# Performance work log

Hardware: AMD Instinct MI355X
Metric: run time of the kernel (lower is better)

Reference implementation:

```python
import jax, jax.numpy as jnp
import numpy as np

B, N, K, D_MODEL = 4, 16384, 32, 64

def gather_neighbors(x, idx):
    # x: [B, N, F], idx: [B, N, K] -> [B, N, K, F]
    return jnp.take_along_axis(x[:, :, None, :], idx[:, :, :, None], axis=1)

def setup_inputs() -> dict:
    key = jax.random.key(0)
    k1, k2, k3, k4, k5 = jax.random.split(key, 5)
    x = jax.random.normal(k1, (B, N, D_MODEL), dtype=jnp.float32)
    pos = jax.random.normal(k2, (B, N, 3), dtype=jnp.float32)
    neighbor_idx = jax.random.randint(k3, (B, N, K), 0, N, dtype=jnp.int32)
    W1 = jax.random.normal(k4, (3, D_MODEL), dtype=jnp.float32) * (1.0 / np.sqrt(3.0))
    b1 = jnp.zeros((D_MODEL,), dtype=jnp.float32)
    W2 = jax.random.normal(k5, (D_MODEL, D_MODEL), dtype=jnp.float32) * (1.0 / np.sqrt(D_MODEL))
    b2 = jnp.zeros((D_MODEL,), dtype=jnp.float32)
    return {"x": x, "pos": pos, "neighbor_idx": neighbor_idx,
            "W1": W1, "b1": b1, "W2": W2, "b2": b2}

def reference(x, pos, neighbor_idx, W1, b1, W2, b2):
    # gather neighbor positions: [B, N, K, 3]
    neighbors = gather_neighbors(pos, neighbor_idx)
    rel_pos = pos[:, :, None, :] - neighbors              # [B, N, K, 3]
    # weight MLP: Linear(3,d) + LeakyReLU(0.1), Linear(d,d)
    h = jax.nn.leaky_relu(jnp.einsum('bnkd,df->bnkf', rel_pos, W1) + b1, 0.1)
    w = jnp.einsum('bnkf,fg->bnkg', h, W2) + b2           # [B, N, K, F]
    xg = gather_neighbors(x, neighbor_idx)                # [B, N, K, F]
    return jnp.sum(w * xg, axis=2)                        # [B, N, F]
```

## Files before the change

### kernel.cpp

```cpp
#include <hip/hip_runtime.h>


#define NPTS   16384
#define KNB    32
#define F      64
#define BATCH  4
#define LOG2N  14
#define WPTS   8

typedef _Float16 h2     __attribute__((ext_vector_type(2)));
typedef _Float16 h8     __attribute__((ext_vector_type(8)));
typedef float    f32x16 __attribute__((ext_vector_type(16)));

__global__ __launch_bounds__(256, 2) void pointconv_mfma(
    const float* __restrict__ x,
    const float* __restrict__ pos,
    const int*   __restrict__ idx,
    const float* __restrict__ W1,
    const float* __restrict__ b1,
    const float* __restrict__ W2,
    const float* __restrict__ b2,
    float*       __restrict__ out)
{
    __shared__ __align__(16) _Float16 w1p[32][8];
    __shared__ __align__(16) _Float16 w2f[2][4][2][32][8];

    const int tid = threadIdx.x;
    if (tid < 32) {
        const int g = 2 * tid;
        w1p[tid][0] = (_Float16)W1[0 * F + g]; w1p[tid][1] = (_Float16)W1[0 * F + g + 1];
        w1p[tid][2] = (_Float16)W1[1 * F + g]; w1p[tid][3] = (_Float16)W1[1 * F + g + 1];
        w1p[tid][4] = (_Float16)W1[2 * F + g]; w1p[tid][5] = (_Float16)W1[2 * F + g + 1];
        w1p[tid][6] = (_Float16)b1[g];         w1p[tid][7] = (_Float16)b1[g + 1];
    }
#pragma unroll
    for (int r = 0; r < 16; ++r) {
        const int e = r * 256 + tid;
        const int g = e >> 6, f = e & 63;
        w2f[(g >> 3) & 1][g >> 4][f & 1][f >> 1][g & 7] = (_Float16)W2[e];
    }
    __syncthreads();

    const int lane = tid & 63;
    const int wv   = tid >> 6;
    const int m    = lane & 31;
    const int hf   = lane >> 5;

    h8 bfrag[4][2];
#pragma unroll
    for (int t = 0; t < 4; ++t)
#pragma unroll
        for (int c = 0; c < 2; ++c)
            bfrag[t][c] = *(const h8*)&w2f[hf][t][c][m][0];

    const float2 b2v = *(const float2*)(b2 + 2 * m);

    const int gb    = blockIdx.x;
    const int xcd   = gb & 7;
    const int q     = gb >> 3;
    const int batch = xcd >> 1;
    const int pg    = q + ((xcd & 1) << 8);
    const int base  = batch << LOG2N;
    const int p0_s  = base + pg * (4 * WPTS) + wv * WPTS;
    const float* __restrict__ xb2 = x + (size_t)base * F + 2 * m;

    int jm;
    float rx, ry, rz;
    {
        jm = idx[p0_s * KNB + m];
        const int nr = base + jm;
        rx = pos[p0_s * 3 + 0] - pos[nr * 3 + 0];
        ry = pos[p0_s * 3 + 1] - pos[nr * 3 + 1];
        rz = pos[p0_s * 3 + 2] - pos[nr * 3 + 2];
    }

    const h2 c01 = { (_Float16)0.1f, (_Float16)0.1f };

#pragma unroll 1
    for (int i = 0; i < WPTS; ++i) {
        const int p_s = p0_s + i;

        float2 xv[16];
#pragma unroll
        for (int reg = 0; reg < 16; ++reg) {
            const int rA = (reg & 3) + ((reg >> 2) << 3) + (hf << 2);
            const int jk = __shfl(jm, rA);
            xv[reg] = *(const float2*)(xb2 + (size_t)jk * F);
        }

        int jmn = 0;
        float rxn = 0.f, ryn = 0.f, rzn = 0.f;
        if (i + 1 < WPTS) {
            jmn = idx[(p_s + 1) * KNB + m];
            const int nr = base + jmn;
            rxn = pos[(p_s + 1) * 3 + 0] - pos[nr * 3 + 0];
            ryn = pos[(p_s + 1) * 3 + 1] - pos[nr * 3 + 1];
            rzn = pos[(p_s + 1) * 3 + 2] - pos[nr * 3 + 2];
        }

        f32x16 acc0, acc1;
#pragma unroll
        for (int r = 0; r < 16; ++r) { acc0[r] = b2v.x; acc1[r] = b2v.y; }

        const h2 rxp = { (_Float16)rx, (_Float16)rx };
        const h2 ryp = { (_Float16)ry, (_Float16)ry };
        const h2 rzp = { (_Float16)rz, (_Float16)rz };

#pragma unroll
        for (int t = 0; t < 4; ++t) {
            h8 af;
#pragma unroll
            for (int jj = 0; jj < 4; ++jj) {
                const int g2 = 8 * t + 4 * hf + jj;
                const h8 w = *(const h8*)&w1p[g2][0];
                const h2 wx = __builtin_shufflevector(w, w, 0, 1);
                const h2 wy = __builtin_shufflevector(w, w, 2, 3);
                const h2 wz = __builtin_shufflevector(w, w, 4, 5);
                const h2 bb = __builtin_shufflevector(w, w, 6, 7);
                h2 hv = bb + rxp * wx;
                hv = hv + ryp * wy;
                hv = hv + rzp * wz;
                hv = __builtin_elementwise_max(hv, hv * c01);
                af[2 * jj]     = hv[0];
                af[2 * jj + 1] = hv[1];
            }
            acc0 = __builtin_amdgcn_mfma_f32_32x32x16_f16(af, bfrag[t][0], acc0, 0, 0, 0);
            acc1 = __builtin_amdgcn_mfma_f32_32x32x16_f16(af, bfrag[t][1], acc1, 0, 0, 0);
        }

        float s0 = 0.f, s1 = 0.f;
#pragma unroll
        for (int reg = 0; reg < 16; ++reg) {
            s0 = fmaf(acc0[reg], xv[reg].x, s0);
            s1 = fmaf(acc1[reg], xv[reg].y, s1);
        }
        s0 += __shfl_xor(s0, 32);
        s1 += __shfl_xor(s1, 32);
        if (hf == 0)
            *(float2*)(out + (size_t)p_s * F + 2 * m) = make_float2(s0, s1);

        jm = jmn; rx = rxn; ry = ryn; rz = rzn;
    }
}

extern "C" void kernel_launch(void* const* d_in, const int* in_sizes, int n_in,
                              void* d_out, int out_size, void* d_ws, size_t ws_size,
                              hipStream_t stream) {
    const float* x   = (const float*)d_in[0];
    const float* pos = (const float*)d_in[1];
    const int*   idx = (const int*)  d_in[2];
    const float* W1  = (const float*)d_in[3];
    const float* b1  = (const float*)d_in[4];
    const float* W2  = (const float*)d_in[5];
    const float* b2  = (const float*)d_in[6];
    float* out = (float*)d_out;

    dim3 grid((BATCH * NPTS) / (4 * WPTS));
    dim3 block(256);
    pointconv_mfma<<<grid, block, 0, stream>>>(x, pos, idx, W1, b1, W2, b2, out);
}
```

Before: 145.3 us.

## Gather neighbor features as float4 rows and reduce via LDS transpose

Each lane now gathers neighbor feature rows as 16-byte float4 loads, one neighbor row per 16-lane group, instead of 8-byte float2 loads spread in the MFMA output layout. The MFMA accumulator results are written to a per-wave LDS tile so they can be read back in the matching float4 layout, multiplied with the gathered features, and reduced with cross-lane shuffles. This halves the number of gather instructions and widens each access. In exchange it adds LDS traffic, about 35 KB of shared memory per block, and extra shuffles. No barrier is placed between the LDS write and read, which relies on intra-wave ordering.

Result: no change. 147.3 us (+1.4%).

```diff
diff --git a/kernel.cpp b/kernel.cpp
--- a/kernel.cpp
+++ b/kernel.cpp
@@ -24,6 +24,7 @@
 {
     __shared__ __align__(16) _Float16 w1p[32][8];
     __shared__ __align__(16) _Float16 w2f[2][4][2][32][8];
+    __shared__ __align__(16) float swave[4][KNB][68];
 
     const int tid = threadIdx.x;
     if (tid < 32) {
@@ -45,6 +46,8 @@
     const int wv   = tid >> 6;
     const int m    = lane & 31;
     const int hf   = lane >> 5;
+    const int q    = lane >> 4;
+    const int fq   = lane & 15;
 
     h8 bfrag[4][2];
 #pragma unroll
@@ -57,12 +60,12 @@
 
     const int gb    = blockIdx.x;
     const int xcd   = gb & 7;
-    const int q     = gb >> 3;
+    const int qq    = gb >> 3;
     const int batch = xcd >> 1;
-    const int pg    = q + ((xcd & 1) << 8);
+    const int pg    = qq + ((xcd & 1) << 8);
     const int base  = batch << LOG2N;
     const int p0_s  = base + pg * (4 * WPTS) + wv * WPTS;
-    const float* __restrict__ xb2 = x + (size_t)base * F + 2 * m;
+    const float* __restrict__ xb4 = x + (size_t)base * F + 4 * fq;
 
     int jm;
     float rx, ry, rz;
@@ -80,12 +83,11 @@
     for (int i = 0; i < WPTS; ++i) {
         const int p_s = p0_s + i;
 
-        float2 xv[16];
+        float4 xs[8];
 #pragma unroll
-        for (int reg = 0; reg < 16; ++reg) {
-            const int rA = (reg & 3) + ((reg >> 2) << 3) + (hf << 2);
-            const int jk = __shfl(jm, rA);
-            xv[reg] = *(const float2*)(xb2 + (size_t)jk * F);
+        for (int c = 0; c < 8; ++c) {
+            const int jr = __shfl(jm, 4 * c + q);
+            xs[c] = *(const float4*)(xb4 + (size_t)jr * F);
         }
 
         int jmn = 0;
@@ -128,16 +130,33 @@
             acc1 = __builtin_amdgcn_mfma_f32_32x32x16_f16(af, bfrag[t][1], acc1, 0, 0, 0);
         }
 
-        float s0 = 0.f, s1 = 0.f;
 #pragma unroll
         for (int reg = 0; reg < 16; ++reg) {
-            s0 = fmaf(acc0[reg], xv[reg].x, s0);
-            s1 = fmaf(acc1[reg], xv[reg].y, s1);
+            const int r = (reg & 3) + ((reg >> 2) << 3) + (hf << 2);
+            *(float2*)&swave[wv][r][2 * m] = make_float2(acc0[reg], acc1[reg]);
         }
-        s0 += __shfl_xor(s0, 32);
-        s1 += __shfl_xor(s1, 32);
-        if (hf == 0)
-            *(float2*)(out + (size_t)p_s * F + 2 * m) = make_float2(s0, s1);
+
+        float4 part = make_float4(0.f, 0.f, 0.f, 0.f);
+#pragma unroll
+        for (int c = 0; c < 8; ++c) {
+            const float4 s4 = *(const float4*)&swave[wv][4 * c + q][4 * fq];
+            part.x = fmaf(s4.x, xs[c].x, part.x);
+            part.y = fmaf(s4.y, xs[c].y, part.y);
+            part.z = fmaf(s4.z, xs[c].z, part.z);
+            part.w = fmaf(s4.w, xs[c].w, part.w);
+        }
+
+        part.x += __shfl_xor(part.x, 16);
+        part.y += __shfl_xor(part.y, 16);
+        part.z += __shfl_xor(part.z, 16);
+        part.w += __shfl_xor(part.w, 16);
+        part.x += __shfl_xor(part.x, 32);
+        part.y += __shfl_xor(part.y, 32);
+        part.z += __shfl_xor(part.z, 32);
+        part.w += __shfl_xor(part.w, 32);
+
+        if (lane < 16)
+            *(float4*)(out + (size_t)p_s * F + 4 * fq) = part;
 
         jm = jmn; rx = rxn; ry = ryn; rz = rzn;
     }
```
